# Kernel optimization log

Hardware: AMD Instinct MI355X
Metric: run time of the kernel (lower is better)

## Reference

```python
import jax, jax.numpy as jnp
import numpy as np


def _primes_below(n):
    primes = []
    for i in range(2, n):
        if all(i % p for p in primes):
            primes.append(i)
    return np.array(primes, dtype=np.int32)  # 168 primes for n=1000

_PRIMES = _primes_below(1000)  # shape (168,)


def setup_inputs() -> dict:
    key = jax.random.key(0)
    k1, k2, k3 = jax.random.split(key, 3)
    B, N = 64, 524288
    x = jax.random.normal(k1, (B, N), dtype=jnp.float32)
    kernel = jax.random.normal(k2, (168, 1000), dtype=jnp.float32)
    bias = jax.random.normal(k3, (168, 1000), dtype=jnp.float32)
    return {"x": x, "kernel": kernel, "bias": bias}


def _prime_mask(weights, n):
    # mask[k] = sum_p weights[p, k mod prime_p]; equivalent to the tf.map_fn
    # tile-and-truncate construct in the original layer.
    pos = jnp.arange(n, dtype=jnp.int32)                    # (N,)
    mods = pos[None, :] % jnp.asarray(_PRIMES)[:, None]     # (168, N)
    gathered = jnp.take_along_axis(weights, mods, axis=1)   # (168, N)
    return gathered.sum(axis=0)                             # (N,)


def reference(x, kernel, bias):
    n = x.shape[1]
    w = _prime_mask(kernel, n)  # (N,)
    b = _prime_mask(bias, n)    # (N,)
    # broadcast over batch, same as expand_dims(..., axis=0) in the original
    return x * w[None, :] + b[None, :]
```

## Files before the change

kernel.cpp:

```cpp
#include <hip/hip_runtime.h>
#include <stdint.h>

#define N_COLS 524288
#define N_ROWS 64
#define N_PRIMES 168
#define BLOCK 256
#define COLS_PER_BLOCK 1024
#define CG_TOTAL (N_COLS / 4)

static constexpr uint32_t PRIMES[N_PRIMES] = {
      2,   3,   5,   7,  11,  13,  17,  19,  23,  29,
     31,  37,  41,  43,  47,  53,  59,  61,  67,  71,
     73,  79,  83,  89,  97, 101, 103, 107, 109, 113,
    127, 131, 137, 139, 149, 151, 157, 163, 167, 173,
    179, 181, 191, 193, 197, 199, 211, 223, 227, 229,
    233, 239, 241, 251, 257, 263, 269, 271, 277, 281,
    283, 293, 307, 311, 313, 317, 331, 337, 347, 349,
    353, 359, 367, 373, 379, 383, 389, 397, 401, 409,
    419, 421, 431, 433, 439, 443, 449, 457, 461, 463,
    467, 479, 487, 491, 499, 503, 509, 521, 523, 541,
    547, 557, 563, 569, 571, 577, 587, 593, 599, 601,
    607, 613, 617, 619, 631, 641, 643, 647, 653, 659,
    661, 673, 677, 683, 691, 701, 709, 719, 727, 733,
    739, 743, 751, 757, 761, 769, 773, 787, 797, 809,
    811, 821, 823, 827, 829, 839, 853, 857, 859, 863,
    877, 881, 883, 887, 907, 911, 919, 929, 937, 941,
    947, 953, 967, 971, 977, 983, 991, 997
};

__global__ __launch_bounds__(BLOCK) void bwl_prime_fused_v2(
    const float* __restrict__ x,
    const float* __restrict__ kern,
    const float* __restrict__ bias,
    float* __restrict__ out)
{
    __shared__ float wl[COLS_PER_BLOCK];
    __shared__ float bl[COLS_PER_BLOCK];

    const int t = threadIdx.x;
    const uint32_t col0 = (uint32_t)blockIdx.x * COLS_PER_BLOCK + (uint32_t)t;

    float w0 = 0.f, w1 = 0.f, w2 = 0.f, w3 = 0.f;
    float b0 = 0.f, b1 = 0.f, b2 = 0.f, b3 = 0.f;

#pragma unroll
    for (int i = 0; i < N_PRIMES; ++i) {
        const uint32_t p = PRIMES[i];
        const int off = i * 1000;
        const uint32_t d = 256u % p;
        uint32_t m = col0 % p;
        w0 += kern[off + (int)m];  b0 += bias[off + (int)m];
        m += d; if (m >= p) m -= p;
        w1 += kern[off + (int)m];  b1 += bias[off + (int)m];
        m += d; if (m >= p) m -= p;
        w2 += kern[off + (int)m];  b2 += bias[off + (int)m];
        m += d; if (m >= p) m -= p;
        w3 += kern[off + (int)m];  b3 += bias[off + (int)m];
    }

    wl[t]       = w0;  bl[t]       = b0;
    wl[t + 256] = w1;  bl[t + 256] = b1;
    wl[t + 512] = w2;  bl[t + 512] = b2;
    wl[t + 768] = w3;  bl[t + 768] = b3;
    __syncthreads();

    const float4 wv = ((const float4*)wl)[t];
    const float4 bv = ((const float4*)bl)[t];

    const int cg = blockIdx.x * BLOCK + t;
    const float4* __restrict__ x4 = (const float4*)x;
    float4* __restrict__ o4 = (float4*)out;

#pragma unroll 8
    for (int r = 0; r < N_ROWS; ++r) {
        const size_t off = (size_t)r * CG_TOTAL + cg;
        float4 xv = x4[off];
        float4 ov;
        ov.x = fmaf(xv.x, wv.x, bv.x);
        ov.y = fmaf(xv.y, wv.y, bv.y);
        ov.z = fmaf(xv.z, wv.z, bv.z);
        ov.w = fmaf(xv.w, wv.w, bv.w);
        o4[off] = ov;
    }
}

extern "C" void kernel_launch(void* const* d_in, const int* in_sizes, int n_in,
                              void* d_out, int out_size, void* d_ws, size_t ws_size,
                              hipStream_t stream) {
    (void)in_sizes; (void)n_in; (void)d_ws; (void)ws_size;
    const float* x    = (const float*)d_in[0];
    const float* kern = (const float*)d_in[1];
    const float* bias = (const float*)d_in[2];
    float* out = (float*)d_out;

    bwl_prime_fused_v2<<<N_COLS / COLS_PER_BLOCK, BLOCK, 0, stream>>>(
        x, kern, bias, out);
}
```

Baseline: 267.6 us.

## Split mask computation into separate kernel and stream rows across 2D grid

Adds a two-kernel path. The first kernel builds the prime-mask weight and bias vectors into workspace memory, one column per thread. The second streams x with a 2D grid that splits the 64 rows into 8 chunks, so many more blocks run and the memory-bound FMA pass gets more parallelism. This costs an extra launch and a workspace round trip; the old fused kernel is kept as a fallback when the workspace is too small.

Measured after the change: 267.0 us. Within noise of the previous version (-0.2%).

```diff
diff --git a/kernel.cpp b/kernel.cpp
--- a/kernel.cpp
+++ b/kernel.cpp
@@ -5,7 +5,7 @@
 #define N_ROWS 64
 #define N_PRIMES 168
 #define BLOCK 256
-#define COLS_PER_BLOCK 1024
+#define ROW_CHUNKS 8
 #define CG_TOTAL (N_COLS / 4)
 
 static constexpr uint32_t PRIMES[N_PRIMES] = {
@@ -28,17 +28,66 @@
     947, 953, 967, 971, 977, 983, 991, 997
 };
 
+__global__ __launch_bounds__(BLOCK) void bwl_prime_mask_v3(
+    const float* __restrict__ kern,
+    const float* __restrict__ bias,
+    float* __restrict__ wsw,
+    float* __restrict__ wsb)
+{
+    const uint32_t col = blockIdx.x * BLOCK + threadIdx.x;
+
+    float w = 0.f, b = 0.f;
+#pragma unroll
+    for (int i = 0; i < N_PRIMES; ++i) {
+        const uint32_t p = PRIMES[i];
+        const int off = i * 1000;
+        const uint32_t m = col % p;
+        w += kern[off + (int)m];
+        b += bias[off + (int)m];
+    }
+    wsw[col] = w;
+    wsb[col] = b;
+}
+
+__global__ __launch_bounds__(BLOCK) void bwl_prime_stream_v3(
+    const float* __restrict__ x,
+    const float4* __restrict__ wsw,
+    const float4* __restrict__ wsb,
+    float* __restrict__ out)
+{
+    const int cg = blockIdx.x * BLOCK + threadIdx.x;
+    const int r0 = blockIdx.y * (N_ROWS / ROW_CHUNKS);
+
+    const float4 w = wsw[cg];
+    const float4 b = wsb[cg];
+
+    const float4* __restrict__ x4 = (const float4*)x;
+    float4* __restrict__ o4 = (float4*)out;
+
+#pragma unroll
+    for (int i = 0; i < N_ROWS / ROW_CHUNKS; ++i) {
+        const size_t off = (size_t)(r0 + i) * CG_TOTAL + cg;
+        float4 xv = x4[off];
+        float4 ov;
+        ov.x = fmaf(xv.x, w.x, b.x);
+        ov.y = fmaf(xv.y, w.y, b.y);
+        ov.z = fmaf(xv.z, w.z, b.z);
+        ov.w = fmaf(xv.w, w.w, b.w);
+        o4[off] = ov;
+    }
+}
+
 __global__ __launch_bounds__(BLOCK) void bwl_prime_fused_v2(
     const float* __restrict__ x,
     const float* __restrict__ kern,
     const float* __restrict__ bias,
     float* __restrict__ out)
 {
-    __shared__ float wl[COLS_PER_BLOCK];
-    __shared__ float bl[COLS_PER_BLOCK];
+    __shared__ float wl[1024];
+    __shared__ float bl[1024];
 
     const int t = threadIdx.x;
-    const uint32_t col0 = (uint32_t)blockIdx.x * COLS_PER_BLOCK + (uint32_t)t;
+    const uint32_t col0 = (uint32_t)blockIdx.x * 1024u + (uint32_t)t;
 
     float w0 = 0.f, w1 = 0.f, w2 = 0.f, w3 = 0.f;
     float b0 = 0.f, b1 = 0.f, b2 = 0.f, b3 = 0.f;
@@ -87,12 +136,26 @@
 extern "C" void kernel_launch(void* const* d_in, const int* in_sizes, int n_in,
                               void* d_out, int out_size, void* d_ws, size_t ws_size,
                               hipStream_t stream) {
-    (void)in_sizes; (void)n_in; (void)d_ws; (void)ws_size;
+    (void)in_sizes; (void)n_in; (void)out_size;
     const float* x    = (const float*)d_in[0];
     const float* kern = (const float*)d_in[1];
     const float* bias = (const float*)d_in[2];
     float* out = (float*)d_out;
 
-    bwl_prime_fused_v2<<<N_COLS / COLS_PER_BLOCK, BLOCK, 0, stream>>>(
-        x, kern, bias, out);
+    const size_t need = (size_t)2 * N_COLS * sizeof(float);
+
+    if (ws_size >= need) {
+        float* wsw = (float*)d_ws;
+        float* wsb = wsw + N_COLS;
+
+        bwl_prime_mask_v3<<<N_COLS / BLOCK, BLOCK, 0, stream>>>(
+            kern, bias, wsw, wsb);
+
+        dim3 sgrid(CG_TOTAL / BLOCK, ROW_CHUNKS);
+        bwl_prime_stream_v3<<<sgrid, BLOCK, 0, stream>>>(
+            x, (const float4*)wsw, (const float4*)wsb, out);
+    } else {
+        bwl_prime_fused_v2<<<N_COLS / 1024, BLOCK, 0, stream>>>(
+            x, kern, bias, out);
+    }
 }
```
